# Kernel tuning notes

Measured on AMD Instinct MI355X. Metric: run time of the kernel, lower is better.

Reference implementation:

```python
import jax, jax.numpy as jnp
import numpy as np

ODE_DIM = 512
BATCH = 32768
N_STEPS = 50  # (T - t0) / dt with dt = (1-0)/(50*n_layers), n_layers=1
DT = 1.0 / N_STEPS


def setup_inputs() -> dict:
    key = jax.random.key(0)
    k_x, k_w, k_b, k_g = jax.random.split(key, 4)
    x = jax.random.normal(k_x, (BATCH, ODE_DIM), dtype=jnp.float32)
    # nn.Linear(ODE_dim, ODE_dim) default init ~ U(-1/sqrt(d), 1/sqrt(d))
    bound = 1.0 / np.sqrt(ODE_DIM)
    W_in = jax.random.uniform(k_w, (ODE_DIM, ODE_DIM), dtype=jnp.float32,
                              minval=-bound, maxval=bound)
    b_in = jax.random.uniform(k_b, (ODE_DIM,), dtype=jnp.float32,
                              minval=-bound, maxval=bound)
    # gamma_layer = bias of an nn.Linear(ODE_dim, ODE_dim)
    gamma = jax.random.uniform(k_g, (ODE_DIM,), dtype=jnp.float32,
                               minval=-bound, maxval=bound)
    return {"x": x, "W_in": W_in, "b_in": b_in, "gamma": gamma}


def reference(x, W_in, b_in, gamma):
    # architecture = 'inside_weights' (-1):
    #   rhs(x) = x @ diag(gamma) + tanh(x @ W_in^T + b_in)
    # diag(gamma) on the right is a per-column elementwise scale.
    def euler_step(state, _):
        rhs = state * gamma + jnp.tanh(state @ W_in.T + b_in)
        return state + DT * rhs, None

    out, _ = jax.lax.scan(euler_step, x, None, length=N_STEPS)
    return out
```

## Files before the change

### kernel.cpp

```cpp
#include <hip/hip_runtime.h>
#include <hip/hip_bf16.h>
#include <cstdint>
#include <cstddef>


#define D_DIM 512
#define BATCH_N 32768
#define NSTEPS 50
#define A_STRIDE 520

typedef __bf16 bf16x8 __attribute__((ext_vector_type(8)));
typedef float f32x4 __attribute__((ext_vector_type(4)));

__device__ __forceinline__ float bf16_bits_to_f(unsigned short u) {
    union { unsigned int i; float f; } c;
    c.i = ((unsigned int)u) << 16;
    return c.f;
}
__device__ __forceinline__ unsigned short f_to_bf16_bits(float f) {
    union { float f; unsigned int i; } c;
    c.f = f;
    unsigned int u = c.i;
    unsigned int r = (u + 0x7fffu + ((u >> 16) & 1u)) >> 16;
    return (unsigned short)r;
}

__global__ __launch_bounds__(256) void build_wperm(
    const float* __restrict__ W, unsigned short* __restrict__ Wb) {
    int e4 = blockIdx.x * 256 + threadIdx.x;
    int k4   = e4 & 127;
    int orow = e4 >> 7;
    int i    = orow & 63;
    int srow = (orow & ~63) | (4 * (i & 15) + (i >> 4));
    float4 v = ((const float4*)W)[srow * 128 + k4];
    ushort4 o;
    o.x = f_to_bf16_bits(v.x);
    o.y = f_to_bf16_bits(v.y);
    o.z = f_to_bf16_bits(v.z);
    o.w = f_to_bf16_bits(v.w);
    ((ushort4*)Wb)[orow * 128 + k4] = o;
}

__global__ __launch_bounds__(512, 2) void node_persist(
    const float* __restrict__ X,
    const unsigned short* __restrict__ Wb,
    const float* __restrict__ bias,
    const float* __restrict__ gamma,
    float* __restrict__ Fout)
{
    __shared__ unsigned short ldsA[64 * A_STRIDE];

    const int tid  = threadIdx.x;
    const int lane = tid & 63;
    const int w    = tid >> 6;
    const int l16  = lane & 15;
    const int quad = lane >> 4;
    const int bm   = blockIdx.x;
    const float dt = 1.0f / 50.0f;

    const int ctrue0 = w * 64 + 4 * l16;

    const unsigned short* bp[4];
#pragma unroll
    for (int t = 0; t < 4; ++t)
        bp[t] = Wb + (size_t)(w * 64 + t * 16 + l16) * D_DIM + quad * 8;

    float bc_[4], g1_[4];
    {
        float4 b4 = *(const float4*)&bias[ctrue0];
        float4 g4 = *(const float4*)&gamma[ctrue0];
        bc_[0] = b4.x; bc_[1] = b4.y; bc_[2] = b4.z; bc_[3] = b4.w;
        g1_[0] = 1.0f + dt * g4.x; g1_[1] = 1.0f + dt * g4.y;
        g1_[2] = 1.0f + dt * g4.z; g1_[3] = 1.0f + dt * g4.w;
    }

    const int r0 = quad * 4;
    float s[4][4][4];
#pragma unroll
    for (int tm = 0; tm < 4; ++tm)
#pragma unroll
        for (int r = 0; r < 4; ++r) {
            float4 v = *(const float4*)
                &X[(size_t)(bm * 64 + r0 + tm * 16 + r) * D_DIM + ctrue0];
            s[tm][0][r] = v.x; s[tm][1][r] = v.y;
            s[tm][2][r] = v.z; s[tm][3][r] = v.w;
        }

#pragma unroll
    for (int tm = 0; tm < 4; ++tm)
#pragma unroll
        for (int r = 0; r < 4; ++r) {
            ushort4 h;
            h.x = f_to_bf16_bits(s[tm][0][r]);
            h.y = f_to_bf16_bits(s[tm][1][r]);
            h.z = f_to_bf16_bits(s[tm][2][r]);
            h.w = f_to_bf16_bits(s[tm][3][r]);
            *(ushort4*)&ldsA[(r0 + tm * 16 + r) * A_STRIDE + ctrue0] = h;
        }

    bf16x8 bf0[4], bf1[4];
#pragma unroll
    for (int t = 0; t < 4; ++t)
        bf0[t] = *reinterpret_cast<const bf16x8*>(bp[t]);

    __syncthreads();

    for (int step = 0; step < NSTEPS; ++step) {
        f32x4 acc[4][4];
#pragma unroll
        for (int tm = 0; tm < 4; ++tm)
#pragma unroll
            for (int tn = 0; tn < 4; ++tn) {
                f32x4 b4 = {bc_[tn], bc_[tn], bc_[tn], bc_[tn]};
                acc[tm][tn] = b4;
            }

#pragma unroll
        for (int kb2 = 0; kb2 < 8; ++kb2) {
            const int kb = kb2 * 2;
#pragma unroll
            for (int t = 0; t < 4; ++t)
                bf1[t] = *reinterpret_cast<const bf16x8*>(
                    bp[t] + ((kb + 1) & 15) * 32);
            {
                bf16x8 af[4];
#pragma unroll
                for (int t = 0; t < 4; ++t)
                    af[t] = *reinterpret_cast<const bf16x8*>(
                        &ldsA[(t * 16 + l16) * A_STRIDE + kb * 32 + quad * 8]);
#pragma unroll
                for (int tm = 0; tm < 4; ++tm)
#pragma unroll
                    for (int tn = 0; tn < 4; ++tn)
                        acc[tm][tn] = __builtin_amdgcn_mfma_f32_16x16x32_bf16(
                            af[tm], bf0[tn], acc[tm][tn], 0, 0, 0);
            }
#pragma unroll
            for (int t = 0; t < 4; ++t)
                bf0[t] = *reinterpret_cast<const bf16x8*>(
                    bp[t] + ((kb + 2) & 15) * 32);
            {
                bf16x8 af[4];
#pragma unroll
                for (int t = 0; t < 4; ++t)
                    af[t] = *reinterpret_cast<const bf16x8*>(
                        &ldsA[(t * 16 + l16) * A_STRIDE + (kb + 1) * 32 + quad * 8]);
#pragma unroll
                for (int tm = 0; tm < 4; ++tm)
#pragma unroll
                    for (int tn = 0; tn < 4; ++tn)
                        acc[tm][tn] = __builtin_amdgcn_mfma_f32_16x16x32_bf16(
                            af[tm], bf1[tn], acc[tm][tn], 0, 0, 0);
            }
        }

#pragma unroll
        for (int tm = 0; tm < 4; ++tm)
#pragma unroll
            for (int tn = 0; tn < 4; ++tn)
#pragma unroll
                for (int r = 0; r < 4; ++r) {
                    float y = acc[tm][tn][r];
                    float e = __expf(2.0f * y);
                    float th = 1.0f - 2.0f * __builtin_amdgcn_rcpf(e + 1.0f);
                    s[tm][tn][r] = s[tm][tn][r] * g1_[tn] + dt * th;
                }

        if (step == NSTEPS - 1) break;

        __syncthreads();
#pragma unroll
        for (int tm = 0; tm < 4; ++tm)
#pragma unroll
            for (int r = 0; r < 4; ++r) {
                ushort4 h;
                h.x = f_to_bf16_bits(s[tm][0][r]);
                h.y = f_to_bf16_bits(s[tm][1][r]);
                h.z = f_to_bf16_bits(s[tm][2][r]);
                h.w = f_to_bf16_bits(s[tm][3][r]);
                *(ushort4*)&ldsA[(r0 + tm * 16 + r) * A_STRIDE + ctrue0] = h;
            }
        __syncthreads();
    }

#pragma unroll
    for (int tm = 0; tm < 4; ++tm)
#pragma unroll
        for (int r = 0; r < 4; ++r) {
            float4 v;
            v.x = s[tm][0][r]; v.y = s[tm][1][r];
            v.z = s[tm][2][r]; v.w = s[tm][3][r];
            *(float4*)&Fout[(size_t)(bm * 64 + r0 + tm * 16 + r) * D_DIM + ctrue0] = v;
        }
}

extern "C" void kernel_launch(void* const* d_in, const int* in_sizes, int n_in,
                              void* d_out, int out_size, void* d_ws, size_t ws_size,
                              hipStream_t stream) {
    const float* x  = (const float*)d_in[0];
    const float* W  = (const float*)d_in[1];
    const float* bi = (const float*)d_in[2];
    const float* ga = (const float*)d_in[3];

    unsigned short* Wb = (unsigned short*)d_ws;

    build_wperm<<<256, 256, 0, stream>>>(W, Wb);
    node_persist<<<dim3(512), dim3(512), 0, stream>>>(
        x, Wb, bi, ga, (float*)d_out);
}
```

Measured before the change: 1.537 ms.

## Halve rows per block and pre-lay W in fragment order for coalesced loads

Each block now handles 32 batch rows instead of 64, launching 1024 blocks with a launch-bounds hint of 4 blocks per CU. That cuts the accumulator and state registers and halves the LDS footprint, aiming for more resident waves to hide global W loads. The W prep kernel now writes bf16 weights in the exact per-lane MFMA fragment order, so each wave's B loads are contiguous 16-byte chunks. The trade-off is half as many MFMAs per W fragment loaded, which doubles the W traffic through L2 per unit of work.

```diff
diff --git a/kernel.cpp b/kernel.cpp
--- a/kernel.cpp
+++ b/kernel.cpp
@@ -1,22 +1,16 @@
 #include <hip/hip_runtime.h>
-#include <hip/hip_bf16.h>
 #include <cstdint>
 #include <cstddef>
 
 
 #define D_DIM 512
-#define BATCH_N 32768
 #define NSTEPS 50
 #define A_STRIDE 520
 
 typedef __bf16 bf16x8 __attribute__((ext_vector_type(8)));
 typedef float f32x4 __attribute__((ext_vector_type(4)));
-
-__device__ __forceinline__ float bf16_bits_to_f(unsigned short u) {
-    union { unsigned int i; float f; } c;
-    c.i = ((unsigned int)u) << 16;
-    return c.f;
-}
+typedef unsigned short ushort8_t __attribute__((ext_vector_type(8)));
+
 __device__ __forceinline__ unsigned short f_to_bf16_bits(float f) {
     union { float f; unsigned int i; } c;
     c.f = f;
@@ -25,30 +19,35 @@
     return (unsigned short)r;
 }
 
-__global__ __launch_bounds__(256) void build_wperm(
-    const float* __restrict__ W, unsigned short* __restrict__ Wb) {
-    int e4 = blockIdx.x * 256 + threadIdx.x;
-    int k4   = e4 & 127;
-    int orow = e4 >> 7;
-    int i    = orow & 63;
-    int srow = (orow & ~63) | (4 * (i & 15) + (i >> 4));
-    float4 v = ((const float4*)W)[srow * 128 + k4];
-    ushort4 o;
-    o.x = f_to_bf16_bits(v.x);
-    o.y = f_to_bf16_bits(v.y);
-    o.z = f_to_bf16_bits(v.z);
-    o.w = f_to_bf16_bits(v.w);
-    ((ushort4*)Wb)[orow * 128 + k4] = o;
-}
-
-__global__ __launch_bounds__(512, 2) void node_persist(
+__global__ __launch_bounds__(256) void build_wl(
+    const float* __restrict__ W, unsigned short* __restrict__ Wl) {
+    int f = blockIdx.x * 256 + threadIdx.x;
+    int quad = f & 3;
+    int l16  = (f >> 2) & 15;
+    int t    = (f >> 6) & 3;
+    int kb   = (f >> 8) & 15;
+    int w    = f >> 12;
+    int i    = t * 16 + l16;
+    int srow = w * 64 + 4 * (i & 15) + (i >> 4);
+    int k0   = kb * 32 + quad * 8;
+    float4 a = *(const float4*)&W[(size_t)srow * D_DIM + k0];
+    float4 b = *(const float4*)&W[(size_t)srow * D_DIM + k0 + 4];
+    ushort8_t o;
+    o[0] = f_to_bf16_bits(a.x); o[1] = f_to_bf16_bits(a.y);
+    o[2] = f_to_bf16_bits(a.z); o[3] = f_to_bf16_bits(a.w);
+    o[4] = f_to_bf16_bits(b.x); o[5] = f_to_bf16_bits(b.y);
+    o[6] = f_to_bf16_bits(b.z); o[7] = f_to_bf16_bits(b.w);
+    *(ushort8_t*)&Wl[(size_t)f * 8] = o;
+}
+
+__global__ __launch_bounds__(512, 4) void node_persist(
     const float* __restrict__ X,
-    const unsigned short* __restrict__ Wb,
+    const unsigned short* __restrict__ Wl,
     const float* __restrict__ bias,
     const float* __restrict__ gamma,
     float* __restrict__ Fout)
 {
-    __shared__ unsigned short ldsA[64 * A_STRIDE];
+    __shared__ unsigned short ldsA[32 * A_STRIDE];
 
     const int tid  = threadIdx.x;
     const int lane = tid & 63;
@@ -60,10 +59,8 @@
 
     const int ctrue0 = w * 64 + 4 * l16;
 
-    const unsigned short* bp[4];
-#pragma unroll
-    for (int t = 0; t < 4; ++t)
-        bp[t] = Wb + (size_t)(w * 64 + t * 16 + l16) * D_DIM + quad * 8;
+    const unsigned short* bpw =
+        Wl + (size_t)w * 32768 + (size_t)(l16 * 4 + quad) * 8;
 
     float bc_[4], g1_[4];
     {
@@ -75,19 +72,19 @@
     }
 
     const int r0 = quad * 4;
-    float s[4][4][4];
-#pragma unroll
-    for (int tm = 0; tm < 4; ++tm)
+    float s[2][4][4];
+#pragma unroll
+    for (int tm = 0; tm < 2; ++tm)
 #pragma unroll
         for (int r = 0; r < 4; ++r) {
             float4 v = *(const float4*)
-                &X[(size_t)(bm * 64 + r0 + tm * 16 + r) * D_DIM + ctrue0];
+                &X[(size_t)(bm * 32 + r0 + tm * 16 + r) * D_DIM + ctrue0];
             s[tm][0][r] = v.x; s[tm][1][r] = v.y;
             s[tm][2][r] = v.z; s[tm][3][r] = v.w;
         }
 
 #pragma unroll
-    for (int tm = 0; tm < 4; ++tm)
+    for (int tm = 0; tm < 2; ++tm)
 #pragma unroll
         for (int r = 0; r < 4; ++r) {
             ushort4 h;
@@ -101,14 +98,14 @@
     bf16x8 bf0[4], bf1[4];
 #pragma unroll
     for (int t = 0; t < 4; ++t)
-        bf0[t] = *reinterpret_cast<const bf16x8*>(bp[t]);
+        bf0[t] = *reinterpret_cast<const bf16x8*>(bpw + t * 512);
 
     __syncthreads();
 
     for (int step = 0; step < NSTEPS; ++step) {
-        f32x4 acc[4][4];
-#pragma unroll
-        for (int tm = 0; tm < 4; ++tm)
+        f32x4 acc[2][4];
+#pragma unroll
+        for (int tm = 0; tm < 2; ++tm)
 #pragma unroll
             for (int tn = 0; tn < 4; ++tn) {
                 f32x4 b4 = {bc_[tn], bc_[tn], bc_[tn], bc_[tn]};
@@ -118,35 +115,39 @@
 #pragma unroll
         for (int kb2 = 0; kb2 < 8; ++kb2) {
             const int kb = kb2 * 2;
-#pragma unroll
-            for (int t = 0; t < 4; ++t)
-                bf1[t] = *reinterpret_cast<const bf16x8*>(
-                    bp[t] + ((kb + 1) & 15) * 32);
-            {
-                bf16x8 af[4];
+            {
+                const unsigned short* bk = bpw + (kb + 1) * 2048;
 #pragma unroll
                 for (int t = 0; t < 4; ++t)
-                    af[t] = *reinterpret_cast<const bf16x8*>(
-                        &ldsA[(t * 16 + l16) * A_STRIDE + kb * 32 + quad * 8]);
-#pragma unroll
-                for (int tm = 0; tm < 4; ++tm)
+                    bf1[t] = *reinterpret_cast<const bf16x8*>(bk + t * 512);
+            }
+            {
+                bf16x8 af[2];
+#pragma unroll
+                for (int tm = 0; tm < 2; ++tm)
+                    af[tm] = *reinterpret_cast<const bf16x8*>(
+                        &ldsA[(tm * 16 + l16) * A_STRIDE + kb * 32 + quad * 8]);
+#pragma unroll
+                for (int tm = 0; tm < 2; ++tm)
 #pragma unroll
                     for (int tn = 0; tn < 4; ++tn)
                         acc[tm][tn] = __builtin_amdgcn_mfma_f32_16x16x32_bf16(
                             af[tm], bf0[tn], acc[tm][tn], 0, 0, 0);
             }
-#pragma unroll
-            for (int t = 0; t < 4; ++t)
-                bf0[t] = *reinterpret_cast<const bf16x8*>(
-                    bp[t] + ((kb + 2) & 15) * 32);
-            {
-                bf16x8 af[4];
+            {
+                const unsigned short* bk = bpw + ((kb + 2) & 15) * 2048;
 #pragma unroll
                 for (int t = 0; t < 4; ++t)
-                    af[t] = *reinterpret_cast<const bf16x8*>(
-                        &ldsA[(t * 16 + l16) * A_STRIDE + (kb + 1) * 32 + quad * 8]);
-#pragma unroll
-                for (int tm = 0; tm < 4; ++tm)
+                    bf0[t] = *reinterpret_cast<const bf16x8*>(bk + t * 512);
+            }
+            {
+                bf16x8 af[2];
+#pragma unroll
+                for (int tm = 0; tm < 2; ++tm)
+                    af[tm] = *reinterpret_cast<const bf16x8*>(
+                        &ldsA[(tm * 16 + l16) * A_STRIDE + (kb + 1) * 32 + quad * 8]);
+#pragma unroll
+                for (int tm = 0; tm < 2; ++tm)
 #pragma unroll
                     for (int tn = 0; tn < 4; ++tn)
                         acc[tm][tn] = __builtin_amdgcn_mfma_f32_16x16x32_bf16(
@@ -155,7 +156,7 @@
         }
 
 #pragma unroll
-        for (int tm = 0; tm < 4; ++tm)
+        for (int tm = 0; tm < 2; ++tm)
 #pragma unroll
             for (int tn = 0; tn < 4; ++tn)
 #pragma unroll
@@ -170,7 +171,7 @@
 
         __syncthreads();
 #pragma unroll
-        for (int tm = 0; tm < 4; ++tm)
+        for (int tm = 0; tm < 2; ++tm)
 #pragma unroll
             for (int r = 0; r < 4; ++r) {
                 ushort4 h;
@@ -184,13 +185,13 @@
     }
 
 #pragma unroll
-    for (int tm = 0; tm < 4; ++tm)
+    for (int tm = 0; tm < 2; ++tm)
 #pragma unroll
         for (int r = 0; r < 4; ++r) {
             float4 v;
             v.x = s[tm][0][r]; v.y = s[tm][1][r];
             v.z = s[tm][2][r]; v.w = s[tm][3][r];
-            *(float4*)&Fout[(size_t)(bm * 64 + r0 + tm * 16 + r) * D_DIM + ctrue0] = v;
+            *(float4*)&Fout[(size_t)(bm * 32 + r0 + tm * 16 + r) * D_DIM + ctrue0] = v;
         }
 }
 
@@ -202,9 +203,9 @@
     const float* bi = (const float*)d_in[2];
     const float* ga = (const float*)d_in[3];
 
-    unsigned short* Wb = (unsigned short*)d_ws;
-
-    build_wperm<<<256, 256, 0, stream>>>(W, Wb);
-    node_persist<<<dim3(512), dim3(512), 0, stream>>>(
-        x, Wb, bi, ga, (float*)d_out);
-}
+    unsigned short* Wl = (unsigned short*)d_ws;
+
+    build_wl<<<128, 256, 0, stream>>>(W, Wl);
+    node_persist<<<dim3(1024), dim3(512), 0, stream>>>(
+        x, Wl, bi, ga, (float*)d_out);
+}
```

Result: slower. 3.765 ms (+144.9%).
